# Kernel optimization log

Hardware: AMD Instinct MI355X
Metric: run time of the kernel (lower is better)

## Reference

```python
import jax, jax.numpy as jnp
import numpy as np

H = 512      # memory_width
LIN = 128    # linear_width
IO = 1       # io_width
DEPTH = 2
L = 8192     # input_length


def setup_inputs() -> dict:
    key = jax.random.key(0)
    ks = jax.random.split(key, 12)
    s = 0.05  # small init scale
    return {
        "input": jax.random.normal(ks[0], (L, IO), jnp.float32),
        "residual": jnp.zeros((1, 1, H), jnp.float32),
        "memory": jnp.zeros((DEPTH, 1, H), jnp.float32),
        "W_proc": jax.random.normal(ks[1], (LIN, IO), jnp.float32) * s,
        "b_proc": jax.random.normal(ks[2], (LIN,), jnp.float32) * s,
        "W_ih0": jax.random.normal(ks[3], (3 * H, LIN), jnp.float32) * s,
        "W_hh0": jax.random.normal(ks[4], (3 * H, H), jnp.float32) * s,
        "b_ih0": jax.random.normal(ks[5], (3 * H,), jnp.float32) * s,
        "b_hh0": jax.random.normal(ks[6], (3 * H,), jnp.float32) * s,
        "W_ih1": jax.random.normal(ks[7], (3 * H, H), jnp.float32) * s,
        "W_hh1": jax.random.normal(ks[8], (3 * H, H), jnp.float32) * s,
        "b_ih1": jax.random.normal(ks[9], (3 * H,), jnp.float32) * s,
        "b_hh1": jax.random.normal(ks[10], (3 * H,), jnp.float32) * s,
        "input_length": L,
    }


def _gru_cell(x, h, Wi, Wh, bi, bh):
    # torch nn.GRU cell: gates ordered (r, z, n)
    gi = Wi @ x + bi
    gh = Wh @ h + bh
    i_r, i_z, i_n = jnp.split(gi, 3)
    h_r, h_z, h_n = jnp.split(gh, 3)
    r = jax.nn.sigmoid(i_r + h_r)
    z = jax.nn.sigmoid(i_z + h_z)
    n = jnp.tanh(i_n + r * h_n)
    return (1.0 - z) * n + z * h


def reference(input, residual, memory, W_proc, b_proc,
              W_ih0, W_hh0, b_ih0, b_hh0,
              W_ih1, W_hh1, b_ih1, b_hh1, input_length):
    def step(carry, x_t):
        h0, h1, res = carry
        p = W_proc @ x_t + b_proc                      # Linear(io_width -> linear_width)
        h0 = _gru_cell(p, h0, W_ih0, W_hh0, b_ih0, b_hh0)
        h1 = _gru_cell(h0, h1, W_ih1, W_hh1, b_ih1, b_hh1)
        res = jax.nn.sigmoid(res + h1)                 # residual += rnn_out; sigmoid
        return (h0, h1, res), None

    carry0 = (memory[0, 0], memory[1, 0], residual[0, 0])
    (h0, h1, res), _ = jax.lax.scan(step, carry0, input[: input_length - 1])
    residual_out = res[None, None, :]                  # (1,1,H)
    memory_out = jnp.stack([h0, h1])[:, None, :]       # (depth,1,H)
    return residual_out, memory_out
```

## Files before the change

kernel.cpp:

```cpp
#include <hip/hip_runtime.h>
#include <math.h>

#define Hh   512
#define TH   1536
#define LINN 128
typedef unsigned long long ull;
typedef unsigned int u32;

#define WS_A     0
#define WS_CC    6144
#define WS_RING0 16384
#define WS_RING1 49152

__device__ __forceinline__ float sigm(float v) { return 1.f / (1.f + __expf(-v)); }
__device__ __forceinline__ float tanh_fast(float x) { return 2.f / (1.f + __expf(-2.f * x)) - 1.f; }
__device__ __forceinline__ ull  pk(float v, u32 tag) { return ((ull)tag << 32) | (ull)__float_as_uint(v); }
__device__ __forceinline__ ull  ring_ld(const ull* p) {
    return __hip_atomic_load(p, __ATOMIC_RELAXED, __HIP_MEMORY_SCOPE_AGENT);
}
__device__ __forceinline__ void ring_st(ull* p, ull v) {
    __hip_atomic_store(p, v, __ATOMIC_RELAXED, __HIP_MEMORY_SCOPE_AGENT);
}

#define SPIN_LD(var, ptr, tag)                                        \
    {                                                                 \
        int _t = 0;                                                   \
        var = ring_ld(ptr);                                           \
        while ((u32)((var) >> 32) < (tag)) {                          \
            if (++_t > 2) __builtin_amdgcn_s_sleep(2);                \
            var = ring_ld(ptr);                                       \
        }                                                             \
    }

__global__ void prep(const float* __restrict__ Wih0, const float* __restrict__ Wproc,
                     const float* __restrict__ bproc, const float* __restrict__ bih0,
                     const float* __restrict__ bhh0, float* __restrict__ A,
                     float* __restrict__ CC)
{
    int row = blockIdx.x * 256 + threadIdx.x;
    if (row >= TH) return;
    const float* w = Wih0 + (size_t)row * LINN;
    float a = 0.f, c = 0.f;
    for (int k = 0; k < LINN; ++k) { float wv = w[k]; a = fmaf(wv, Wproc[k], a); c = fmaf(wv, bproc[k], c); }
    c += bih0[row];
    if (row < 2 * Hh) c += bhh0[row];
    A[row] = a; CC[row] = c;
}

__global__ void ringinit(const float* __restrict__ mem, ull* __restrict__ ring0,
                         ull* __restrict__ ring1)
{
    const int t = threadIdx.x;
    for (int slot = 0; slot < 8; ++slot) {
        ring0[slot * Hh + t] = pk(slot == 7 ? mem[t]      : 0.f, 0u);
        ring1[slot * Hh + t] = pk(slot == 7 ? mem[Hh + t] : 0.f, 0u);
    }
}

__launch_bounds__(256, 1)
__global__ void fused(const float* __restrict__ input, const float* __restrict__ resid,
                      const float* __restrict__ Whh0, const float* __restrict__ bhh0,
                      const float* __restrict__ A, const float* __restrict__ CC,
                      const float* __restrict__ Wih1, const float* __restrict__ Whh1,
                      const float* __restrict__ bih1, const float* __restrict__ bhh1,
                      ull* __restrict__ ring0, ull* __restrict__ ring1,
                      float* __restrict__ outp, int T)
{
    __shared__ __align__(16) float smem[13312];
    const int tid = threadIdx.x;
    const int wg  = blockIdx.x;

    if (wg < 64) {
        float* Wl = smem;
        float* hl = smem + 12288;
        const int jl = tid >> 5;
        const int s2 = tid & 31;
        const int jg = wg * 8 + jl;
        for (int i = tid; i < 24 * Hh; i += 256) {
            int lr = i >> 9, k = i & (Hh - 1);
            int g = lr % 3, j = lr / 3;
            Wl[i] = Whh0[(size_t)(g * Hh + wg * 8 + j) * Hh + k];
        }
        const float Ar = A[jg], Az = A[jg + Hh], An = A[jg + 2 * Hh];
        const float Cr = CC[jg], Cz = CC[jg + Hh], Cn = CC[jg + 2 * Hh];
        const float Bn = bhh0[jg + 2 * Hh];
        const float4* W4 = (const float4*)Wl;
        __syncthreads();

        for (int s = 0; s < T; ++s) {
            if (tid == 0 && s >= 7) {
                const ull* bp = ring1 + (size_t)((s - 7) & 7) * Hh;
                ull b;
                SPIN_LD(b, bp, (u32)(s - 6));
            }
            const ull* base = ring0 + (size_t)((s - 1) & 7) * Hh;
            const u32 tgt = (u32)s;
            ull w0, w1;
            SPIN_LD(w0, base + tid, tgt);
            SPIN_LD(w1, base + tid + 256, tgt);
            __syncthreads();
            hl[tid]       = __uint_as_float((u32)w0);
            hl[tid + 256] = __uint_as_float((u32)w1);
            __syncthreads();
            const float x = input[s];
            const float4* hb4 = (const float4*)hl;
            float4 hv[4];
#pragma unroll
            for (int c = 0; c < 4; ++c) hv[c] = hb4[s2 + 32 * c];
            float acc[3];
#pragma unroll
            for (int g = 0; g < 3; ++g) {
                const float4* Wr = W4 + (jl * 3 + g) * 128;
                float a = 0.f;
#pragma unroll
                for (int c = 0; c < 4; ++c) {
                    const float4 w = Wr[s2 + 32 * c], h = hv[c];
                    a = fmaf(w.x, h.x, a); a = fmaf(w.y, h.y, a);
                    a = fmaf(w.z, h.z, a); a = fmaf(w.w, h.w, a);
                }
                acc[g] = a;
            }
#pragma unroll
            for (int o = 16; o > 0; o >>= 1) {
                acc[0] += __shfl_xor(acc[0], o);
                acc[1] += __shfl_xor(acc[1], o);
                acc[2] += __shfl_xor(acc[2], o);
            }
            if (s2 == 0) {
                const float r  = sigm(fmaf(Ar, x, Cr) + acc[0]);
                const float z  = sigm(fmaf(Az, x, Cz) + acc[1]);
                const float n  = tanh_fast(fmaf(An, x, Cn) + r * (acc[2] + Bn));
                const float hn = (1.f - z) * n + z * hl[jg];
                ring_st(ring0 + (size_t)(s & 7) * Hh + jg, pk(hn, (u32)(s + 1)));
                if (s == T - 1) outp[Hh + jg] = hn;
            }
        }
    } else {
        float* Wl  = smem;
        float* hl0 = smem + 12288;
        float* hl1 = smem + 12800;
        const int w  = tid >> 6;
        const int l  = tid & 63;
        const int jg = (wg - 64) * 4 + w;
        for (int i = tid; i < 24 * Hh; i += 256) {
            int lr = i >> 9, k = i & (Hh - 1);
            int ww = lr / 6, q = lr % 6;
            int hj = (wg - 64) * 4 + ww;
            const float* src = (q < 3) ? &Wih1[(size_t)(q * Hh + hj) * Hh]
                                       : &Whh1[(size_t)((q - 3) * Hh + hj) * Hh];
            Wl[i] = src[k];
        }
        const float Br  = bih1[jg] + bhh1[jg];
        const float Bz  = bih1[jg + Hh] + bhh1[jg + Hh];
        const float Bin = bih1[jg + 2 * Hh];
        const float Bhn = bhh1[jg + 2 * Hh];
        const float4* W4 = (const float4*)Wl;
        float resl = resid[jg];
        __syncthreads();

        for (int u = 0; u < T; ++u) {
            const ull* b0 = ring0 + (size_t)(u & 7) * Hh;
            const ull* b1 = ring1 + (size_t)((u - 1) & 7) * Hh;
            const u32 t0g = (u32)(u + 1), t1g = (u32)u;
            ull a0, a1, c0, c1;
            SPIN_LD(a0, b0 + tid, t0g);
            SPIN_LD(a1, b0 + tid + 256, t0g);
            SPIN_LD(c0, b1 + tid, t1g);
            SPIN_LD(c1, b1 + tid + 256, t1g);
            __syncthreads();
            hl0[tid]       = __uint_as_float((u32)a0);
            hl0[tid + 256] = __uint_as_float((u32)a1);
            hl1[tid]       = __uint_as_float((u32)c0);
            hl1[tid + 256] = __uint_as_float((u32)c1);
            __syncthreads();
            const float4* h04 = (const float4*)hl0;
            const float4* h14 = (const float4*)hl1;
            float4 x0[2], x1[2];
#pragma unroll
            for (int c = 0; c < 2; ++c) { x0[c] = h04[l + 64 * c]; x1[c] = h14[l + 64 * c]; }
            float ai[3], ah[3];
#pragma unroll
            for (int g = 0; g < 3; ++g) {
                const float4* Wi = W4 + (w * 6 + g) * 128;
                const float4* Wh = W4 + (w * 6 + 3 + g) * 128;
                float s1 = 0.f, s2v = 0.f;
#pragma unroll
                for (int c = 0; c < 2; ++c) {
                    const float4 wi = Wi[l + 64 * c], wh = Wh[l + 64 * c];
                    s1  = fmaf(wi.x, x0[c].x, s1);  s1  = fmaf(wi.y, x0[c].y, s1);
                    s1  = fmaf(wi.z, x0[c].z, s1);  s1  = fmaf(wi.w, x0[c].w, s1);
                    s2v = fmaf(wh.x, x1[c].x, s2v); s2v = fmaf(wh.y, x1[c].y, s2v);
                    s2v = fmaf(wh.z, x1[c].z, s2v); s2v = fmaf(wh.w, x1[c].w, s2v);
                }
                ai[g] = s1; ah[g] = s2v;
            }
#pragma unroll
            for (int o = 32; o > 0; o >>= 1) {
                ai[0] += __shfl_xor(ai[0], o); ai[1] += __shfl_xor(ai[1], o); ai[2] += __shfl_xor(ai[2], o);
                ah[0] += __shfl_xor(ah[0], o); ah[1] += __shfl_xor(ah[1], o); ah[2] += __shfl_xor(ah[2], o);
            }
            if (l == 0) {
                const float r   = sigm(ai[0] + ah[0] + Br);
                const float z   = sigm(ai[1] + ah[1] + Bz);
                const float n   = tanh_fast(ai[2] + Bin + r * (ah[2] + Bhn));
                const float h1n = (1.f - z) * n + z * hl1[jg];
                ring_st(ring1 + (size_t)(u & 7) * Hh + jg, pk(h1n, (u32)(u + 1)));
                resl = sigm(resl + h1n);
                if (u == T - 1) { outp[jg] = resl; outp[2 * Hh + jg] = h1n; }
            }
        }
    }
}

extern "C" void kernel_launch(void* const* d_in, const int* in_sizes, int n_in,
                              void* d_out, int out_size, void* d_ws, size_t ws_size,
                              hipStream_t stream)
{
    const float* input    = (const float*)d_in[0];
    const float* residual = (const float*)d_in[1];
    const float* memory   = (const float*)d_in[2];
    const float* Wproc    = (const float*)d_in[3];
    const float* bproc    = (const float*)d_in[4];
    const float* Wih0     = (const float*)d_in[5];
    const float* Whh0     = (const float*)d_in[6];
    const float* bih0     = (const float*)d_in[7];
    const float* bhh0     = (const float*)d_in[8];
    const float* Wih1     = (const float*)d_in[9];
    const float* Whh1     = (const float*)d_in[10];
    const float* bih1     = (const float*)d_in[11];
    const float* bhh1     = (const float*)d_in[12];
    const int L = in_sizes[0];
    const int T = L - 1;
    float* out = (float*)d_out;
    char* ws = (char*)d_ws;

    float* A     = (float*)(ws + WS_A);
    float* CC    = (float*)(ws + WS_CC);
    ull*   ring0 = (ull*)(ws + WS_RING0);
    ull*   ring1 = (ull*)(ws + WS_RING1);

    prep<<<dim3((TH + 255) / 256), dim3(256), 0, stream>>>(Wih0, Wproc, bproc, bih0, bhh0, A, CC);
    ringinit<<<dim3(1), dim3(512), 0, stream>>>(memory, ring0, ring1);
    fused<<<dim3(192), dim3(256), 0, stream>>>(input, residual, Whh0, bhh0, A, CC,
                                               Wih1, Whh1, bih1, bhh1,
                                               ring0, ring1, out, T);
}
```

Baseline: 18.75 ms.

## Store layer-1 GRU weights as bf16 in LDS and halve layer-1 workgroups

Layer-1 workgroups now keep their Wih1/Whh1 rows in shared memory as bf16 instead of fp32. That lets each workgroup own 8 hidden units (32 lanes each) instead of 4, so the grid drops from 192 to 128 workgroups and fewer blocks take part in the per-step spin synchronisation. The spin order is also changed to poll the older layer-1 ring before the layer-0 ring. In exchange, weight precision falls to bf16, which may shift results over the 8191-step recurrence.

After: 29.16 ms. 55.5% more time.

```diff
diff --git a/kernel.cpp b/kernel.cpp
--- a/kernel.cpp
+++ b/kernel.cpp
@@ -6,6 +6,7 @@
 #define LINN 128
 typedef unsigned long long ull;
 typedef unsigned int u32;
+typedef unsigned short u16;
 
 #define WS_A     0
 #define WS_CC    6144
@@ -21,6 +22,13 @@
 __device__ __forceinline__ void ring_st(ull* p, ull v) {
     __hip_atomic_store(p, v, __ATOMIC_RELAXED, __HIP_MEMORY_SCOPE_AGENT);
 }
+__device__ __forceinline__ u16  f2bf(float v) {
+    u32 u = __float_as_uint(v);
+    u32 r = u + 0x7fffu + ((u >> 16) & 1u);
+    return (u16)(r >> 16);
+}
+__device__ __forceinline__ float bflo(u32 p) { return __uint_as_float(p << 16); }
+__device__ __forceinline__ float bfhi(u32 p) { return __uint_as_float(p & 0xffff0000u); }
 
 #define SPIN_LD(var, ptr, tag)                                        \
     {                                                                 \
@@ -136,25 +144,25 @@
             }
         }
     } else {
-        float* Wl  = smem;
+        u16*   Ws  = (u16*)smem;
         float* hl0 = smem + 12288;
         float* hl1 = smem + 12800;
-        const int w  = tid >> 6;
-        const int l  = tid & 63;
-        const int jg = (wg - 64) * 4 + w;
-        for (int i = tid; i < 24 * Hh; i += 256) {
+        const int wg1 = wg - 64;
+        const int hh  = tid >> 5;
+        const int s2  = tid & 31;
+        const int jg  = wg1 * 8 + hh;
+        for (int i = tid; i < 48 * Hh; i += 256) {
             int lr = i >> 9, k = i & (Hh - 1);
-            int ww = lr / 6, q = lr % 6;
-            int hj = (wg - 64) * 4 + ww;
+            int hw = lr / 6, q = lr % 6;
+            int hj = wg1 * 8 + hw;
             const float* src = (q < 3) ? &Wih1[(size_t)(q * Hh + hj) * Hh]
                                        : &Whh1[(size_t)((q - 3) * Hh + hj) * Hh];
-            Wl[i] = src[k];
+            Ws[lr * Hh + k] = f2bf(src[k]);
         }
         const float Br  = bih1[jg] + bhh1[jg];
         const float Bz  = bih1[jg + Hh] + bhh1[jg + Hh];
         const float Bin = bih1[jg + 2 * Hh];
         const float Bhn = bhh1[jg + 2 * Hh];
-        const float4* W4 = (const float4*)Wl;
         float resl = resid[jg];
         __syncthreads();
 
@@ -163,10 +171,10 @@
             const ull* b1 = ring1 + (size_t)((u - 1) & 7) * Hh;
             const u32 t0g = (u32)(u + 1), t1g = (u32)u;
             ull a0, a1, c0, c1;
+            SPIN_LD(c0, b1 + tid, t1g);
+            SPIN_LD(c1, b1 + tid + 256, t1g);
             SPIN_LD(a0, b0 + tid, t0g);
             SPIN_LD(a1, b0 + tid + 256, t0g);
-            SPIN_LD(c0, b1 + tid, t1g);
-            SPIN_LD(c1, b1 + tid + 256, t1g);
             __syncthreads();
             hl0[tid]       = __uint_as_float((u32)a0);
             hl0[tid + 256] = __uint_as_float((u32)a1);
@@ -175,31 +183,33 @@
             __syncthreads();
             const float4* h04 = (const float4*)hl0;
             const float4* h14 = (const float4*)hl1;
-            float4 x0[2], x1[2];
-#pragma unroll
-            for (int c = 0; c < 2; ++c) { x0[c] = h04[l + 64 * c]; x1[c] = h14[l + 64 * c]; }
+            float4 x0[4], x1[4];
+#pragma unroll
+            for (int c = 0; c < 4; ++c) { x0[c] = h04[s2 + 32 * c]; x1[c] = h14[s2 + 32 * c]; }
             float ai[3], ah[3];
 #pragma unroll
             for (int g = 0; g < 3; ++g) {
-                const float4* Wi = W4 + (w * 6 + g) * 128;
-                const float4* Wh = W4 + (w * 6 + 3 + g) * 128;
+                const uint2* Wi = (const uint2*)(Ws + (size_t)(hh * 6 + g) * Hh);
+                const uint2* Wh = (const uint2*)(Ws + (size_t)(hh * 6 + 3 + g) * Hh);
                 float s1 = 0.f, s2v = 0.f;
 #pragma unroll
-                for (int c = 0; c < 2; ++c) {
-                    const float4 wi = Wi[l + 64 * c], wh = Wh[l + 64 * c];
-                    s1  = fmaf(wi.x, x0[c].x, s1);  s1  = fmaf(wi.y, x0[c].y, s1);
-                    s1  = fmaf(wi.z, x0[c].z, s1);  s1  = fmaf(wi.w, x0[c].w, s1);
-                    s2v = fmaf(wh.x, x1[c].x, s2v); s2v = fmaf(wh.y, x1[c].y, s2v);
-                    s2v = fmaf(wh.z, x1[c].z, s2v); s2v = fmaf(wh.w, x1[c].w, s2v);
+                for (int c = 0; c < 4; ++c) {
+                    const uint2 wi = Wi[s2 + 32 * c];
+                    const uint2 wh = Wh[s2 + 32 * c];
+                    const float4 v0 = x0[c], v1 = x1[c];
+                    s1  = fmaf(bflo(wi.x), v0.x, s1);  s1  = fmaf(bfhi(wi.x), v0.y, s1);
+                    s1  = fmaf(bflo(wi.y), v0.z, s1);  s1  = fmaf(bfhi(wi.y), v0.w, s1);
+                    s2v = fmaf(bflo(wh.x), v1.x, s2v); s2v = fmaf(bfhi(wh.x), v1.y, s2v);
+                    s2v = fmaf(bflo(wh.y), v1.z, s2v); s2v = fmaf(bfhi(wh.y), v1.w, s2v);
                 }
                 ai[g] = s1; ah[g] = s2v;
             }
 #pragma unroll
-            for (int o = 32; o > 0; o >>= 1) {
+            for (int o = 16; o > 0; o >>= 1) {
                 ai[0] += __shfl_xor(ai[0], o); ai[1] += __shfl_xor(ai[1], o); ai[2] += __shfl_xor(ai[2], o);
                 ah[0] += __shfl_xor(ah[0], o); ah[1] += __shfl_xor(ah[1], o); ah[2] += __shfl_xor(ah[2], o);
             }
-            if (l == 0) {
+            if (s2 == 0) {
                 const float r   = sigm(ai[0] + ah[0] + Br);
                 const float z   = sigm(ai[1] + ah[1] + Bz);
                 const float n   = tanh_fast(ai[2] + Bin + r * (ah[2] + Bhn));
@@ -241,7 +251,7 @@
 
     prep<<<dim3((TH + 255) / 256), dim3(256), 0, stream>>>(Wih0, Wproc, bproc, bih0, bhh0, A, CC);
     ringinit<<<dim3(1), dim3(512), 0, stream>>>(memory, ring0, ring1);
-    fused<<<dim3(192), dim3(256), 0, stream>>>(input, residual, Whh0, bhh0, A, CC,
+    fused<<<dim3(128), dim3(256), 0, stream>>>(input, residual, Whh0, bhh0, A, CC,
                                                Wih1, Whh1, bih1, bhh1,
                                                ring0, ring1, out, T);
 }
```

## Pack layer-0 hidden state as bf16 pairs in the inter-block ring

Applied to the files above, without the earlier changes.

Layer-0 hidden values are now rounded to bf16 and two are packed with the step tag into each 64-bit ring entry. This halves the ring0 buffer and leaves each thread one spin-load per step instead of two. The goal is to cut latency and traffic on the serial per-step handoff between workgroups. The trade-off is that h0 is quantized to bf16 every step and feeds back into the recurrence, so error can build up over the 8191 steps.

After: 31.82 ms. +69.7%, slower.

```diff
diff --git a/kernel.cpp b/kernel.cpp
--- a/kernel.cpp
+++ b/kernel.cpp
@@ -6,11 +6,12 @@
 #define LINN 128
 typedef unsigned long long ull;
 typedef unsigned int u32;
+typedef unsigned short u16;
 
 #define WS_A     0
 #define WS_CC    6144
 #define WS_RING0 16384
-#define WS_RING1 49152
+#define WS_RING1 32768
 
 __device__ __forceinline__ float sigm(float v) { return 1.f / (1.f + __expf(-v)); }
 __device__ __forceinline__ float tanh_fast(float x) { return 2.f / (1.f + __expf(-2.f * x)) - 1.f; }
@@ -20,6 +21,10 @@
 }
 __device__ __forceinline__ void ring_st(ull* p, ull v) {
     __hip_atomic_store(p, v, __ATOMIC_RELAXED, __HIP_MEMORY_SCOPE_AGENT);
+}
+__device__ __forceinline__ u32 f2bf(float v) {
+    u32 u = __float_as_uint(v);
+    return ((u + 0x7fffu + ((u >> 16) & 1u)) >> 16) & 0xffffu;
 }
 
 #define SPIN_LD(var, ptr, tag)                                        \
@@ -52,7 +57,11 @@
 {
     const int t = threadIdx.x;
     for (int slot = 0; slot < 8; ++slot) {
-        ring0[slot * Hh + t] = pk(slot == 7 ? mem[t]      : 0.f, 0u);
+        if (t < 256) {
+            float e = (slot == 7) ? mem[2 * t]     : 0.f;
+            float o = (slot == 7) ? mem[2 * t + 1] : 0.f;
+            ring0[slot * 256 + t] = (ull)((f2bf(e) << 16) | f2bf(o));
+        }
         ring1[slot * Hh + t] = pk(slot == 7 ? mem[Hh + t] : 0.f, 0u);
     }
 }
@@ -93,14 +102,18 @@
                 ull b;
                 SPIN_LD(b, bp, (u32)(s - 6));
             }
-            const ull* base = ring0 + (size_t)((s - 1) & 7) * Hh;
+            const ull* base = ring0 + (size_t)((s - 1) & 7) * 256;
             const u32 tgt = (u32)s;
-            ull w0, w1;
+            ull w0;
             SPIN_LD(w0, base + tid, tgt);
-            SPIN_LD(w1, base + tid + 256, tgt);
-            __syncthreads();
-            hl[tid]       = __uint_as_float((u32)w0);
-            hl[tid + 256] = __uint_as_float((u32)w1);
+            __syncthreads();
+            {
+                const u32 lo = (u32)w0;
+                float2 hv2;
+                hv2.x = __uint_as_float(lo & 0xffff0000u);
+                hv2.y = __uint_as_float(lo << 16);
+                ((float2*)hl)[tid] = hv2;
+            }
             __syncthreads();
             const float x = input[s];
             const float4* hb4 = (const float4*)hl;
@@ -131,7 +144,12 @@
                 const float z  = sigm(fmaf(Az, x, Cz) + acc[1]);
                 const float n  = tanh_fast(fmaf(An, x, Cn) + r * (acc[2] + Bn));
                 const float hn = (1.f - z) * n + z * hl[jg];
-                ring_st(ring0 + (size_t)(s & 7) * Hh + jg, pk(hn, (u32)(s + 1)));
+                const float hn_hi = __shfl(hn, 32);
+                if ((tid & 63) == 0) {
+                    const u32 lo = (f2bf(hn) << 16) | f2bf(hn_hi);
+                    ring_st(ring0 + (size_t)(s & 7) * 256 + wg * 4 + (tid >> 6),
+                            ((ull)(u32)(s + 1) << 32) | (ull)lo);
+                }
                 if (s == T - 1) outp[Hh + jg] = hn;
             }
         }
@@ -159,19 +177,23 @@
         __syncthreads();
 
         for (int u = 0; u < T; ++u) {
-            const ull* b0 = ring0 + (size_t)(u & 7) * Hh;
+            const ull* b0 = ring0 + (size_t)(u & 7) * 256;
             const ull* b1 = ring1 + (size_t)((u - 1) & 7) * Hh;
             const u32 t0g = (u32)(u + 1), t1g = (u32)u;
-            ull a0, a1, c0, c1;
-            SPIN_LD(a0, b0 + tid, t0g);
-            SPIN_LD(a1, b0 + tid + 256, t0g);
+            ull c0, c1, a0;
             SPIN_LD(c0, b1 + tid, t1g);
             SPIN_LD(c1, b1 + tid + 256, t1g);
-            __syncthreads();
-            hl0[tid]       = __uint_as_float((u32)a0);
-            hl0[tid + 256] = __uint_as_float((u32)a1);
+            SPIN_LD(a0, b0 + tid, t0g);
+            __syncthreads();
             hl1[tid]       = __uint_as_float((u32)c0);
             hl1[tid + 256] = __uint_as_float((u32)c1);
+            {
+                const u32 lo = (u32)a0;
+                float2 hv2;
+                hv2.x = __uint_as_float(lo & 0xffff0000u);
+                hv2.y = __uint_as_float(lo << 16);
+                ((float2*)hl0)[tid] = hv2;
+            }
             __syncthreads();
             const float4* h04 = (const float4*)hl0;
             const float4* h14 = (const float4*)hl1;
```
